# Optimization experiments

Measured on AMD Instinct MI355X. Metric: run time of the kernel, lower is better.

Reference implementation:

```python
import jax, jax.numpy as jnp
import numpy as np

N = 100000      # nodes
E = 1_600_000   # edges
IN = 128        # in_channels
HID = 32        # hidden_channels (per head)
HEADS = 4
NC = 10         # num_classes
NEG_SLOPE = 0.2 # GATConv leaky relu slope
BN_EPS = 1e-5


def _gat_conv(x, src, dst, W, a_src, a_dst, bias, heads, out_ch, concat):
    # x: [N, F_in]; W: [F_in, heads*out_ch]; a_src/a_dst: [heads, out_ch]
    n = x.shape[0]
    h = (x @ W).reshape(n, heads, out_ch)                    # [N,H,C]
    al_src = jnp.sum(h * a_src, axis=-1)                     # [N,H]
    al_dst = jnp.sum(h * a_dst, axis=-1)                     # [N,H]
    e = jax.nn.leaky_relu(al_src[src] + al_dst[dst], NEG_SLOPE)  # [E,H]
    # segment softmax over destination node
    m = jax.ops.segment_max(e, dst, num_segments=n)          # [N,H]
    ex = jnp.exp(e - m[dst])
    s = jax.ops.segment_sum(ex, dst, num_segments=n)         # [N,H]
    alpha = ex / (s[dst] + 1e-16)                            # [E,H]
    out = jax.ops.segment_sum(h[src] * alpha[:, :, None], dst, num_segments=n)  # [N,H,C]
    if concat:
        out = out.reshape(n, heads * out_ch)
    else:
        out = out.mean(axis=1)
    return out + bias


def _bn(x, gamma, beta, mean, var):
    # eval-mode BatchNorm1d with running stats
    return (x - mean) * jax.lax.rsqrt(var + BN_EPS) * gamma + beta


def setup_inputs() -> dict:
    key = jax.random.key(0)
    ks = iter(jax.random.split(key, 40))
    d = {}
    d['x'] = jax.random.normal(next(ks), (N, IN), dtype=jnp.float32)
    d['edge_index'] = jax.random.randint(next(ks), (2, E), 0, N, dtype=jnp.int32)
    dims = [(IN, HID, HEADS), (HID * HEADS, HID, HEADS), (HID * HEADS, HID, 1)]
    for i, (fin, c, h) in enumerate(dims):
        d[f'W{i}'] = jax.random.normal(next(ks), (fin, h * c), dtype=jnp.float32) * (1.0 / np.sqrt(fin))
        d[f'as{i}'] = jax.random.normal(next(ks), (h, c), dtype=jnp.float32) * 0.1
        d[f'ad{i}'] = jax.random.normal(next(ks), (h, c), dtype=jnp.float32) * 0.1
        bdim = h * c if i < 2 else c
        d[f'b{i}'] = jnp.zeros((bdim,), dtype=jnp.float32)
        d[f'g{i}'] = jax.random.uniform(next(ks), (bdim,), dtype=jnp.float32, minval=0.5, maxval=1.5)
        d[f'bt{i}'] = jax.random.normal(next(ks), (bdim,), dtype=jnp.float32) * 0.1
        d[f'm{i}'] = jax.random.normal(next(ks), (bdim,), dtype=jnp.float32) * 0.1
        d[f'v{i}'] = jax.random.uniform(next(ks), (bdim,), dtype=jnp.float32, minval=0.5, maxval=1.5)
    d['Wc'] = jax.random.normal(next(ks), (HID, NC), dtype=jnp.float32) * (1.0 / np.sqrt(HID))
    d['bc'] = jnp.zeros((NC,), dtype=jnp.float32)
    return d


def reference(x, edge_index, W0, as0, ad0, b0, g0, bt0, m0, v0,
              W1, as1, ad1, b1, g1, bt1, m1, v1,
              W2, as2, ad2, b2, g2, bt2, m2, v2, Wc, bc):
    src, dst = edge_index[0], edge_index[1]
    # layer 0: concat heads
    h = _gat_conv(x, src, dst, W0, as0, ad0, b0, HEADS, HID, True)
    h = jax.nn.elu(_bn(h, g0, bt0, m0, v0))
    # layer 1: concat heads
    h = _gat_conv(h, src, dst, W1, as1, ad1, b1, HEADS, HID, True)
    h = jax.nn.elu(_bn(h, g1, bt1, m1, v1))
    # layer 2: single head, no concat
    h = _gat_conv(h, src, dst, W2, as2, ad2, b2, 1, HID, False)
    h = jax.nn.elu(_bn(h, g2, bt2, m2, v2))
    # dropout is identity in eval mode
    return h @ Wc + bc
```

## Files before the change

kernel.cpp:

```cpp
#include <hip/hip_runtime.h>
#include <hip/hip_bf16.h>
#include <math.h>

#define NN   100000
#define NE   1600000
#define FIN  128
#define HID  32
#define NHEADS 4
#define NCLS 10

typedef unsigned int uint32;
typedef __fp16 half2_t __attribute__((ext_vector_type(2)));
typedef __fp16 half8_t __attribute__((ext_vector_type(8)));
typedef float  f32x4   __attribute__((ext_vector_type(4)));
typedef uint32 u32x4   __attribute__((ext_vector_type(4)));

__device__ __forceinline__ uint32 packh2(float a, float b) {
    half2_t h = __builtin_amdgcn_cvt_pkrtz(a, b);
    return __builtin_bit_cast(uint32, h);
}
__device__ __forceinline__ float h_lo(uint32 v) {
    return (float)__builtin_bit_cast(half2_t, v)[0];
}
__device__ __forceinline__ float h_hi(uint32 v) {
    return (float)__builtin_bit_cast(half2_t, v)[1];
}
__device__ __forceinline__ half8_t as_h8(uint4 v) {
    return __builtin_bit_cast(half8_t, v);
}

__global__ void zero_i32(int* __restrict__ p, int n) {
    int i = blockIdx.x * blockDim.x + threadIdx.x;
    if (i < n) p[i] = 0;
}

__global__ void hist_rank_kernel(const int* __restrict__ dst, int* __restrict__ cnt,
                                 int* __restrict__ rank, int e) {
    const int t0 = blockIdx.x * (blockDim.x * 4) + threadIdx.x;
    int d[4];
    bool a[4];
#pragma unroll
    for (int k = 0; k < 4; ++k) {
        const int j = t0 + k * 256;
        a[k] = (j < e);
        d[k] = a[k] ? __builtin_nontemporal_load(&dst[j]) : 0;
    }
    int r[4];
#pragma unroll
    for (int k = 0; k < 4; ++k)
        if (a[k]) r[k] = atomicAdd(&cnt[d[k]], 1);
#pragma unroll
    for (int k = 0; k < 4; ++k) {
        const int j = t0 + k * 256;
        if (a[k]) __builtin_nontemporal_store(r[k], &rank[j]);
    }
}

__global__ void scan_block_sums(const int* __restrict__ cnt, int* __restrict__ bsum, int n) {
    __shared__ int sm[256];
    int i = blockIdx.x * 256 + threadIdx.x;
    int v = (i < n) ? cnt[i] : 0;
    sm[threadIdx.x] = v;
    __syncthreads();
    for (int off = 128; off > 0; off >>= 1) {
        if (threadIdx.x < off) sm[threadIdx.x] += sm[threadIdx.x + off];
        __syncthreads();
    }
    if (threadIdx.x == 0) bsum[blockIdx.x] = sm[0];
}

__global__ void scan_single(const int* __restrict__ bsum, int* __restrict__ boff, int nb) {
    __shared__ int sm[512];
    int t = threadIdx.x;
    int v = (t < nb) ? bsum[t] : 0;
    sm[t] = v;
    __syncthreads();
    for (int off = 1; off < 512; off <<= 1) {
        int u = (t >= off) ? sm[t - off] : 0;
        __syncthreads();
        sm[t] += u;
        __syncthreads();
    }
    if (t < nb) boff[t] = sm[t] - v;
}

__global__ void scan_final(const int* __restrict__ cnt, const int* __restrict__ boff,
                           int* __restrict__ rowptr, int n) {
    __shared__ int sm[256];
    int i = blockIdx.x * 256 + threadIdx.x;
    int v = (i < n) ? cnt[i] : 0;
    sm[threadIdx.x] = v;
    __syncthreads();
    for (int off = 1; off < 256; off <<= 1) {
        int u = (threadIdx.x >= off) ? sm[threadIdx.x - off] : 0;
        __syncthreads();
        sm[threadIdx.x] += u;
        __syncthreads();
    }
    int incl = sm[threadIdx.x];
    int excl = incl - v;
    if (i < n) rowptr[i] = boff[blockIdx.x] + excl;
    if (i == n - 1) rowptr[n] = boff[blockIdx.x] + incl;
}

__global__ void scatter_kernel(const int* __restrict__ src, const int* __restrict__ dst,
                               const int* __restrict__ rank, const int* __restrict__ rowptr,
                               int* __restrict__ esrc, int e) {
    const int t0 = blockIdx.x * (blockDim.x * 4) + threadIdx.x;
#pragma unroll
    for (int k = 0; k < 4; ++k) {
        const int j = t0 + k * 256;
        if (j < e) {
            const int d = __builtin_nontemporal_load(&dst[j]);
            const int s = __builtin_nontemporal_load(&src[j]);
            const int r = __builtin_nontemporal_load(&rank[j]);
            __builtin_nontemporal_store(s, &esrc[rowptr[d] + r]);
        }
    }
}

__global__ void conv_w_kernel(const float* __restrict__ W0, const float* __restrict__ W1,
                              const float* __restrict__ W2, uint32* __restrict__ Wt0,
                              uint32* __restrict__ Wt1, uint32* __restrict__ Wt2) {
    int t = blockIdx.x * blockDim.x + threadIdx.x;
    if (t < 8192) {
        const int nn = t >> 6, ku = t & 63;
        Wt0[t] = packh2(W0[(2 * ku) * 128 + nn], W0[(2 * ku + 1) * 128 + nn]);
    } else if (t < 16384) {
        const int l = t - 8192;
        const int nn = l >> 6, ku = l & 63;
        Wt1[l] = packh2(W1[(2 * ku) * 128 + nn], W1[(2 * ku + 1) * 128 + nn]);
    } else if (t < 18432) {
        const int l = t - 16384;
        const int nn = l >> 6, ku = l & 63;
        Wt2[l] = packh2(W2[(2 * ku) * 32 + nn], W2[(2 * ku + 1) * 32 + nn]);
    }
}

__global__ void bn_prep_kernel(
    const float* __restrict__ b0, const float* __restrict__ g0, const float* __restrict__ bt0,
    const float* __restrict__ m0, const float* __restrict__ v0,
    const float* __restrict__ b1, const float* __restrict__ g1, const float* __restrict__ bt1,
    const float* __restrict__ m1, const float* __restrict__ v1,
    const float* __restrict__ b2, const float* __restrict__ g2, const float* __restrict__ bt2,
    const float* __restrict__ m2, const float* __restrict__ v2,
    float* __restrict__ A, float* __restrict__ B) {
    const int t = threadIdx.x;
    const float *b, *g, *bt, *m, *v;
    int c;
    if (t < 128)      { b = b0; g = g0; bt = bt0; m = m0; v = v0; c = t; }
    else if (t < 256) { b = b1; g = g1; bt = bt1; m = m1; v = v1; c = t - 128; }
    else if (t < 288) { b = b2; g = g2; bt = bt2; m = m2; v = v2; c = t - 256; }
    else return;
    const float s = g[c] * rsqrtf(v[c] + 1e-5f);
    A[t] = s;
    B[t] = bt[c] + (b[c] - m[c]) * s;
}

template <int FOUT, int H, bool CONVA>
__global__ __launch_bounds__(256) void gemm_mfma(const void* __restrict__ Xv,
                                                 const uint32* __restrict__ Wt,
                                                 const float* __restrict__ a_s,
                                                 const float* __restrict__ a_d,
                                                 float* __restrict__ alS,
                                                 float* __restrict__ alD,
                                                 uint32* __restrict__ Outh, int n) {
    constexpr int NT = FOUT / 16;
    const int wave = threadIdx.x >> 6;
    const int lane = threadIdx.x & 63;
    const int c = lane & 15;
    const int q = lane >> 4;
    const int row0 = blockIdx.x * 128 + wave * 32;

    int r0 = row0 + c;
    int r1 = row0 + 16 + c;
    if (r0 >= n) r0 = n - 1;
    if (r1 >= n) r1 = n - 1;

    f32x4 acc[2][NT];
#pragma unroll
    for (int m = 0; m < 2; ++m)
#pragma unroll
        for (int nt = 0; nt < NT; ++nt) acc[m][nt] = (f32x4){0.f, 0.f, 0.f, 0.f};

    const uint4*  XU = (const uint4*)Xv;
    const float4* XF = (const float4*)Xv;
    const uint4*  WU = (const uint4*)Wt;

#pragma unroll
    for (int ks = 0; ks < 4; ++ks) {
        half8_t a0, a1;
        if constexpr (CONVA) {
            const float4 f0 = XF[(size_t)r0 * 32 + (ks * 4 + q) * 2];
            const float4 f1 = XF[(size_t)r0 * 32 + (ks * 4 + q) * 2 + 1];
            a0 = as_h8(make_uint4(packh2(f0.x, f0.y), packh2(f0.z, f0.w),
                                  packh2(f1.x, f1.y), packh2(f1.z, f1.w)));
            const float4 g0 = XF[(size_t)r1 * 32 + (ks * 4 + q) * 2];
            const float4 g1 = XF[(size_t)r1 * 32 + (ks * 4 + q) * 2 + 1];
            a1 = as_h8(make_uint4(packh2(g0.x, g0.y), packh2(g0.z, g0.w),
                                  packh2(g1.x, g1.y), packh2(g1.z, g1.w)));
        } else {
            a0 = as_h8(XU[(size_t)r0 * 16 + ks * 4 + q]);
            a1 = as_h8(XU[(size_t)r1 * 16 + ks * 4 + q]);
        }
#pragma unroll
        for (int nt = 0; nt < NT; ++nt) {
            const half8_t b = as_h8(WU[(nt * 16 + c) * 16 + ks * 4 + q]);
            acc[0][nt] = __builtin_amdgcn_mfma_f32_16x16x32_f16(a0, b, acc[0][nt], 0, 0, 0);
            acc[1][nt] = __builtin_amdgcn_mfma_f32_16x16x32_f16(a1, b, acc[1][nt], 0, 0, 0);
        }
    }

    float asv[NT], adv[NT];
#pragma unroll
    for (int nt = 0; nt < NT; ++nt) {
        asv[nt] = a_s[c + 16 * nt];
        adv[nt] = a_d[c + 16 * nt];
    }

#pragma unroll
    for (int m = 0; m < 2; ++m) {
#pragma unroll
        for (int reg = 0; reg < 4; ++reg) {
            const int grow = row0 + m * 16 + q * 4 + reg;
            const bool ok = (grow < n);
            if constexpr (H == 4) {
                float ps[4], pd[4];
#pragma unroll
                for (int h = 0; h < 4; ++h) {
                    ps[h] = acc[m][2 * h][reg] * asv[2 * h] + acc[m][2 * h + 1][reg] * asv[2 * h + 1];
                    pd[h] = acc[m][2 * h][reg] * adv[2 * h] + acc[m][2 * h + 1][reg] * adv[2 * h + 1];
                }
#pragma unroll
                for (int off = 1; off < 16; off <<= 1) {
#pragma unroll
                    for (int h = 0; h < 4; ++h) {
                        ps[h] += __shfl_xor(ps[h], off);
                        pd[h] += __shfl_xor(pd[h], off);
                    }
                }
                if (c < 4 && ok) {
                    const float vs = (c == 0) ? ps[0] : (c == 1) ? ps[1] : (c == 2) ? ps[2] : ps[3];
                    const float vd = (c == 0) ? pd[0] : (c == 1) ? pd[1] : (c == 2) ? pd[2] : pd[3];
                    alS[(size_t)grow * 4 + c] = vs;
                    alD[(size_t)grow * 4 + c] = vd;
                }
            } else {
                float ps = acc[m][0][reg] * asv[0] + acc[m][1][reg] * asv[1];
                float pd = acc[m][0][reg] * adv[0] + acc[m][1][reg] * adv[1];
#pragma unroll
                for (int off = 1; off < 16; off <<= 1) {
                    ps += __shfl_xor(ps, off);
                    pd += __shfl_xor(pd, off);
                }
                if (c == 0 && ok) {
                    alS[grow] = ps;
                    alD[grow] = pd;
                }
            }
#pragma unroll
            for (int nt = 0; nt < NT; ++nt) {
                const float v = acc[m][nt][reg];
                const float o = __shfl_xor(v, 1);
                if (((c & 1) == 0) && ok) {
                    Outh[(size_t)grow * (FOUT / 2) + nt * 8 + (c >> 1)] = packh2(v, o);
                }
            }
        }
    }
}

template <int H, int C>
__global__ __launch_bounds__(256) void gat_aggregate(
    const uint32* __restrict__ Hb,
    const int* __restrict__ rowptr, const int* __restrict__ esrc,
    const float* __restrict__ alS, const float* __restrict__ alD,
    const float* __restrict__ bnA, const float* __restrict__ bnB,
    uint32* __restrict__ B16, int n) {
    constexpr int F    = H * C;
    constexpr int RU4  = F / 8;
    constexpr int SLOTS = 64 / RU4;
    constexpr int UNROLL = 16 / SLOTS;

    const int wave = threadIdx.x >> 6;
    const int lane = threadIdx.x & 63;
    int d = blockIdx.x * 4 + wave;
    if (d >= n) return;
    d = __builtin_amdgcn_readfirstlane(d);

    const int li = lane & (RU4 - 1);
    const int g  = lane / RU4;
    const int head = (H == 4) ? (li >> 2) : 0;

    const float ald = alD[(size_t)d * H + head];
    const int beg = rowptr[d];
    const int end = rowptr[d + 1];
    const int endm1 = end - 1;

    float acc[8];
#pragma unroll
    for (int k = 0; k < 8; ++k) acc[k] = 0.f;
    float den = 0.f;

    const uint4* HbU4 = (const uint4*)Hb;

    for (int base = beg; base < end; base += 16) {
#pragma unroll
        for (int u = 0; u < UNROLL; ++u) {
            const int j  = base + u * SLOTS + g;
            const bool act = (j < end);
            const int jc = act ? j : endm1;
            const int sj = __builtin_nontemporal_load(&esrc[jc]);
            const float aw = (H == 4) ? alS[(size_t)sj * 4 + head] : alS[sj];
            float t = aw + ald;
            t = fmaxf(t, 0.2f * t);
            const float ex = act ? __expf(t) : 0.f;
            den += ex;
            const uint4 v = HbU4[(size_t)sj * RU4 + li];
            acc[0] = fmaf(h_lo(v.x), ex, acc[0]);
            acc[1] = fmaf(h_hi(v.x), ex, acc[1]);
            acc[2] = fmaf(h_lo(v.y), ex, acc[2]);
            acc[3] = fmaf(h_hi(v.y), ex, acc[3]);
            acc[4] = fmaf(h_lo(v.z), ex, acc[4]);
            acc[5] = fmaf(h_hi(v.z), ex, acc[5]);
            acc[6] = fmaf(h_lo(v.w), ex, acc[6]);
            acc[7] = fmaf(h_hi(v.w), ex, acc[7]);
        }
    }

#pragma unroll
    for (int off = RU4; off < 64; off <<= 1) {
#pragma unroll
        for (int k = 0; k < 8; ++k) acc[k] += __shfl_xor(acc[k], off);
        den += __shfl_xor(den, off);
    }

    if (lane < RU4) {
        const float inv = 1.f / (den + 1e-16f);
        const int c0 = 8 * li;
        const float4 A0 = *(const float4*)(bnA + c0);
        const float4 A1 = *(const float4*)(bnA + c0 + 4);
        const float4 B0 = *(const float4*)(bnB + c0);
        const float4 B1 = *(const float4*)(bnB + c0 + 4);
        const float As[8] = {A0.x, A0.y, A0.z, A0.w, A1.x, A1.y, A1.z, A1.w};
        const float Bs[8] = {B0.x, B0.y, B0.z, B0.w, B1.x, B1.y, B1.z, B1.w};
        float y[8];
#pragma unroll
        for (int k = 0; k < 8; ++k) {
            const float yy = acc[k] * inv * As[k] + Bs[k];
            y[k] = yy > 0.f ? yy : expm1f(yy);
        }
        u32x4 o;
        o.x = packh2(y[0], y[1]);
        o.y = packh2(y[2], y[3]);
        o.z = packh2(y[4], y[5]);
        o.w = packh2(y[6], y[7]);
        __builtin_nontemporal_store(o, (u32x4*)B16 + (size_t)d * RU4 + li);
    }
}

__global__ __launch_bounds__(256) void classifier_kernel(
    const uint32* __restrict__ H3, const float* __restrict__ Wc,
    const float* __restrict__ bc, float* __restrict__ out, int n) {
    const int ni = blockIdx.x * blockDim.x + threadIdx.x;
    if (ni >= n) return;
    const uint4* row = (const uint4*)(H3 + (size_t)ni * 16);
    float xf[32];
#pragma unroll
    for (int u = 0; u < 4; ++u) {
        const uint4 v = row[u];
        xf[u * 8 + 0] = h_lo(v.x); xf[u * 8 + 1] = h_hi(v.x);
        xf[u * 8 + 2] = h_lo(v.y); xf[u * 8 + 3] = h_hi(v.y);
        xf[u * 8 + 4] = h_lo(v.z); xf[u * 8 + 5] = h_hi(v.z);
        xf[u * 8 + 6] = h_lo(v.w); xf[u * 8 + 7] = h_hi(v.w);
    }
    float o[NCLS];
#pragma unroll
    for (int c = 0; c < NCLS; ++c) o[c] = bc[c];
#pragma unroll
    for (int u = 0; u < 32; ++u) {
#pragma unroll
        for (int c = 0; c < NCLS; ++c) o[c] = fmaf(xf[u], Wc[u * NCLS + c], o[c]);
    }
    float* orow = out + (size_t)ni * NCLS;
#pragma unroll
    for (int c = 0; c < NCLS; c += 2) {
        *(float2*)(orow + c) = make_float2(o[c], o[c + 1]);
    }
}

static inline char* align256(char* p) {
    return (char*)(((uintptr_t)p + 255) & ~(uintptr_t)255);
}

extern "C" void kernel_launch(void* const* d_in, const int* in_sizes, int n_in,
                              void* d_out, int out_size, void* d_ws, size_t ws_size,
                              hipStream_t stream) {
    const float* x  = (const float*)d_in[0];
    const int*   ei = (const int*)d_in[1];
    const int N = in_sizes[0] / FIN;
    const int E = in_sizes[1] / 2;
    const int* src = ei;
    const int* dst = ei + E;

    const float *W0 = (const float*)d_in[2],  *as0 = (const float*)d_in[3],
                *ad0 = (const float*)d_in[4], *b0 = (const float*)d_in[5],
                *g0 = (const float*)d_in[6],  *bt0 = (const float*)d_in[7],
                *m0 = (const float*)d_in[8],  *v0 = (const float*)d_in[9];
    const float *W1 = (const float*)d_in[10], *as1 = (const float*)d_in[11],
                *ad1 = (const float*)d_in[12],*b1 = (const float*)d_in[13],
                *g1 = (const float*)d_in[14], *bt1 = (const float*)d_in[15],
                *m1 = (const float*)d_in[16], *v1 = (const float*)d_in[17];
    const float *W2 = (const float*)d_in[18], *as2 = (const float*)d_in[19],
                *ad2 = (const float*)d_in[20],*b2 = (const float*)d_in[21],
                *g2 = (const float*)d_in[22], *bt2 = (const float*)d_in[23],
                *m2 = (const float*)d_in[24], *v2 = (const float*)d_in[25];
    const float *Wc = (const float*)d_in[26], *bc = (const float*)d_in[27];
    float* out = (float*)d_out;

    char* p = (char*)d_ws;
    uint32* Ht  = (uint32*)p;   p = align256(p + (size_t)N * 64 * 4);
    uint32* B16 = (uint32*)p;   p = align256(p + (size_t)N * 64 * 4);
    uint32* Wt0 = (uint32*)p;   p = align256(p + 8192 * 4);
    uint32* Wt1 = (uint32*)p;   p = align256(p + 8192 * 4);
    uint32* Wt2 = (uint32*)p;   p = align256(p + 2048 * 4);
    float* alS = (float*)p;     p = align256(p + (size_t)N * NHEADS * 4);
    float* alD = (float*)p;     p = align256(p + (size_t)N * NHEADS * 4);
    int* cnt = (int*)p;         p = align256(p + (size_t)N * 4);
    int* rowptr = (int*)p;      p = align256(p + (size_t)(N + 1) * 4);
    int* rank = (int*)p;        p = align256(p + (size_t)E * 4);
    int* esrc = (int*)p;        p = align256(p + (size_t)E * 4);
    int* bsum = (int*)p;        p = align256(p + 512 * 4);
    int* boff = (int*)p;        p = align256(p + 512 * 4);
    float* bnA = (float*)p;     p = align256(p + 288 * 4);
    float* bnB = (float*)p;     p = align256(p + 288 * 4);
    (void)ws_size; (void)n_in; (void)out_size;

    const int NB = (N + 255) / 256;
    const int EB4 = (E + 1023) / 1024;

    zero_i32<<<NB, 256, 0, stream>>>(cnt, N);
    hist_rank_kernel<<<EB4, 256, 0, stream>>>(dst, cnt, rank, E);
    scan_block_sums<<<NB, 256, 0, stream>>>(cnt, bsum, N);
    scan_single<<<1, 512, 0, stream>>>(bsum, boff, NB);
    scan_final<<<NB, 256, 0, stream>>>(cnt, boff, rowptr, N);
    scatter_kernel<<<EB4, 256, 0, stream>>>(src, dst, rank, rowptr, esrc, E);

    conv_w_kernel<<<72, 256, 0, stream>>>(W0, W1, W2, Wt0, Wt1, Wt2);
    bn_prep_kernel<<<1, 320, 0, stream>>>(b0, g0, bt0, m0, v0,
                                          b1, g1, bt1, m1, v1,
                                          b2, g2, bt2, m2, v2, bnA, bnB);

    const int GB = (N + 127) / 128;
    const int AB = (N + 3) / 4;

    gemm_mfma<128, 4, true><<<GB, 256, 0, stream>>>(x, Wt0, as0, ad0, alS, alD, Ht, N);
    gat_aggregate<4, 32><<<AB, 256, 0, stream>>>(Ht, rowptr, esrc, alS, alD,
                                                 bnA, bnB, B16, N);
    gemm_mfma<128, 4, false><<<GB, 256, 0, stream>>>(B16, Wt1, as1, ad1, alS, alD, Ht, N);
    gat_aggregate<4, 32><<<AB, 256, 0, stream>>>(Ht, rowptr, esrc, alS, alD,
                                                 bnA + 128, bnB + 128, B16, N);
    gemm_mfma<32, 1, false><<<GB, 256, 0, stream>>>(B16, Wt2, as2, ad2, alS, alD, Ht, N);
    gat_aggregate<1, 32><<<AB, 256, 0, stream>>>(Ht, rowptr, esrc, alS, alD,
                                                 bnA + 256, bnB + 256, B16, N);
    classifier_kernel<<<(N + 255) / 256, 256, 0, stream>>>(B16, Wc, bc, out, N);
}
```

Before: 557.9 us.

## Fuse setup kernels, drop rank array, use atomic write pointers in CSR scatter

Merges zeroing, weight conversion and BN parameter prep into one setup kernel, and folds the single-block offset scan into scan_final by having each block sum the preceding block totals. The histogram no longer records per-edge ranks; the scatter instead claims slots with atomics on a per-node write pointer, which removes the 1.6M-entry rank array and its traffic. Non-temporal loads and stores in the aggregation kernel become ordinary accesses. Edge order within each CSR row becomes nondeterministic, which can change floating-point summation order, and the scatter now contends on atomics.

```diff
diff --git a/kernel.cpp b/kernel.cpp
--- a/kernel.cpp
+++ b/kernel.cpp
@@ -13,7 +13,6 @@
 typedef __fp16 half2_t __attribute__((ext_vector_type(2)));
 typedef __fp16 half8_t __attribute__((ext_vector_type(8)));
 typedef float  f32x4   __attribute__((ext_vector_type(4)));
-typedef uint32 u32x4   __attribute__((ext_vector_type(4)));
 
 __device__ __forceinline__ uint32 packh2(float a, float b) {
     half2_t h = __builtin_amdgcn_cvt_pkrtz(a, b);
@@ -29,100 +28,20 @@
     return __builtin_bit_cast(half8_t, v);
 }
 
-__global__ void zero_i32(int* __restrict__ p, int n) {
-    int i = blockIdx.x * blockDim.x + threadIdx.x;
-    if (i < n) p[i] = 0;
-}
-
-__global__ void hist_rank_kernel(const int* __restrict__ dst, int* __restrict__ cnt,
-                                 int* __restrict__ rank, int e) {
-    const int t0 = blockIdx.x * (blockDim.x * 4) + threadIdx.x;
-    int d[4];
-    bool a[4];
-#pragma unroll
-    for (int k = 0; k < 4; ++k) {
-        const int j = t0 + k * 256;
-        a[k] = (j < e);
-        d[k] = a[k] ? __builtin_nontemporal_load(&dst[j]) : 0;
-    }
-    int r[4];
-#pragma unroll
-    for (int k = 0; k < 4; ++k)
-        if (a[k]) r[k] = atomicAdd(&cnt[d[k]], 1);
-#pragma unroll
-    for (int k = 0; k < 4; ++k) {
-        const int j = t0 + k * 256;
-        if (a[k]) __builtin_nontemporal_store(r[k], &rank[j]);
-    }
-}
-
-__global__ void scan_block_sums(const int* __restrict__ cnt, int* __restrict__ bsum, int n) {
-    __shared__ int sm[256];
-    int i = blockIdx.x * 256 + threadIdx.x;
-    int v = (i < n) ? cnt[i] : 0;
-    sm[threadIdx.x] = v;
-    __syncthreads();
-    for (int off = 128; off > 0; off >>= 1) {
-        if (threadIdx.x < off) sm[threadIdx.x] += sm[threadIdx.x + off];
-        __syncthreads();
-    }
-    if (threadIdx.x == 0) bsum[blockIdx.x] = sm[0];
-}
-
-__global__ void scan_single(const int* __restrict__ bsum, int* __restrict__ boff, int nb) {
-    __shared__ int sm[512];
-    int t = threadIdx.x;
-    int v = (t < nb) ? bsum[t] : 0;
-    sm[t] = v;
-    __syncthreads();
-    for (int off = 1; off < 512; off <<= 1) {
-        int u = (t >= off) ? sm[t - off] : 0;
-        __syncthreads();
-        sm[t] += u;
-        __syncthreads();
-    }
-    if (t < nb) boff[t] = sm[t] - v;
-}
-
-__global__ void scan_final(const int* __restrict__ cnt, const int* __restrict__ boff,
-                           int* __restrict__ rowptr, int n) {
-    __shared__ int sm[256];
-    int i = blockIdx.x * 256 + threadIdx.x;
-    int v = (i < n) ? cnt[i] : 0;
-    sm[threadIdx.x] = v;
-    __syncthreads();
-    for (int off = 1; off < 256; off <<= 1) {
-        int u = (threadIdx.x >= off) ? sm[threadIdx.x - off] : 0;
-        __syncthreads();
-        sm[threadIdx.x] += u;
-        __syncthreads();
-    }
-    int incl = sm[threadIdx.x];
-    int excl = incl - v;
-    if (i < n) rowptr[i] = boff[blockIdx.x] + excl;
-    if (i == n - 1) rowptr[n] = boff[blockIdx.x] + incl;
-}
-
-__global__ void scatter_kernel(const int* __restrict__ src, const int* __restrict__ dst,
-                               const int* __restrict__ rank, const int* __restrict__ rowptr,
-                               int* __restrict__ esrc, int e) {
-    const int t0 = blockIdx.x * (blockDim.x * 4) + threadIdx.x;
-#pragma unroll
-    for (int k = 0; k < 4; ++k) {
-        const int j = t0 + k * 256;
-        if (j < e) {
-            const int d = __builtin_nontemporal_load(&dst[j]);
-            const int s = __builtin_nontemporal_load(&src[j]);
-            const int r = __builtin_nontemporal_load(&rank[j]);
-            __builtin_nontemporal_store(s, &esrc[rowptr[d] + r]);
-        }
-    }
-}
-
-__global__ void conv_w_kernel(const float* __restrict__ W0, const float* __restrict__ W1,
-                              const float* __restrict__ W2, uint32* __restrict__ Wt0,
-                              uint32* __restrict__ Wt1, uint32* __restrict__ Wt2) {
-    int t = blockIdx.x * blockDim.x + threadIdx.x;
+__global__ __launch_bounds__(256) void setup_kernel(
+    int* __restrict__ cnt, int n,
+    const float* __restrict__ W0, const float* __restrict__ W1,
+    const float* __restrict__ W2, uint32* __restrict__ Wt0,
+    uint32* __restrict__ Wt1, uint32* __restrict__ Wt2,
+    const float* __restrict__ b0, const float* __restrict__ g0, const float* __restrict__ bt0,
+    const float* __restrict__ m0, const float* __restrict__ v0,
+    const float* __restrict__ b1, const float* __restrict__ g1, const float* __restrict__ bt1,
+    const float* __restrict__ m1, const float* __restrict__ v1,
+    const float* __restrict__ b2, const float* __restrict__ g2, const float* __restrict__ bt2,
+    const float* __restrict__ m2, const float* __restrict__ v2,
+    float* __restrict__ A, float* __restrict__ B) {
+    const int t = blockIdx.x * 256 + threadIdx.x;
+    if (t < n) cnt[t] = 0;
     if (t < 8192) {
         const int nn = t >> 6, ku = t & 63;
         Wt0[t] = packh2(W0[(2 * ku) * 128 + nn], W0[(2 * ku + 1) * 128 + nn]);
@@ -134,27 +53,88 @@
         const int l = t - 16384;
         const int nn = l >> 6, ku = l & 63;
         Wt2[l] = packh2(W2[(2 * ku) * 32 + nn], W2[(2 * ku + 1) * 32 + nn]);
-    }
-}
-
-__global__ void bn_prep_kernel(
-    const float* __restrict__ b0, const float* __restrict__ g0, const float* __restrict__ bt0,
-    const float* __restrict__ m0, const float* __restrict__ v0,
-    const float* __restrict__ b1, const float* __restrict__ g1, const float* __restrict__ bt1,
-    const float* __restrict__ m1, const float* __restrict__ v1,
-    const float* __restrict__ b2, const float* __restrict__ g2, const float* __restrict__ bt2,
-    const float* __restrict__ m2, const float* __restrict__ v2,
-    float* __restrict__ A, float* __restrict__ B) {
+    } else if (t < 18432 + 288) {
+        const int u = t - 18432;
+        const float *b, *g, *bt, *m, *v;
+        int c;
+        if (u < 128)      { b = b0; g = g0; bt = bt0; m = m0; v = v0; c = u; }
+        else if (u < 256) { b = b1; g = g1; bt = bt1; m = m1; v = v1; c = u - 128; }
+        else              { b = b2; g = g2; bt = bt2; m = m2; v = v2; c = u - 256; }
+        const float s = g[c] * rsqrtf(v[c] + 1e-5f);
+        A[u] = s;
+        B[u] = bt[c] + (b[c] - m[c]) * s;
+    }
+}
+
+__global__ void hist_kernel(const int* __restrict__ dst, int* __restrict__ cnt, int e) {
+    const int t0 = blockIdx.x * (blockDim.x * 4) + threadIdx.x;
+#pragma unroll
+    for (int k = 0; k < 4; ++k) {
+        const int j = t0 + k * 256;
+        if (j < e) atomicAdd(&cnt[dst[j]], 1);
+    }
+}
+
+__global__ void scan_block_sums(const int* __restrict__ cnt, int* __restrict__ bsum, int n) {
+    __shared__ int sm[256];
+    int i = blockIdx.x * 256 + threadIdx.x;
+    int v = (i < n) ? cnt[i] : 0;
+    sm[threadIdx.x] = v;
+    __syncthreads();
+    for (int off = 128; off > 0; off >>= 1) {
+        if (threadIdx.x < off) sm[threadIdx.x] += sm[threadIdx.x + off];
+        __syncthreads();
+    }
+    if (threadIdx.x == 0) bsum[blockIdx.x] = sm[0];
+}
+
+__global__ void scan_final(const int* __restrict__ cnt, const int* __restrict__ bsum,
+                           int* __restrict__ rowptr, int* __restrict__ wptr, int n) {
+    __shared__ int sm[256];
+    const int b = blockIdx.x;
     const int t = threadIdx.x;
-    const float *b, *g, *bt, *m, *v;
-    int c;
-    if (t < 128)      { b = b0; g = g0; bt = bt0; m = m0; v = v0; c = t; }
-    else if (t < 256) { b = b1; g = g1; bt = bt1; m = m1; v = v1; c = t - 128; }
-    else if (t < 288) { b = b2; g = g2; bt = bt2; m = m2; v = v2; c = t - 256; }
-    else return;
-    const float s = g[c] * rsqrtf(v[c] + 1e-5f);
-    A[t] = s;
-    B[t] = bt[c] + (b[c] - m[c]) * s;
+    int s = 0;
+    for (int i = t; i < b; i += 256) s += bsum[i];
+    sm[t] = s;
+    __syncthreads();
+    for (int off = 128; off > 0; off >>= 1) {
+        if (t < off) sm[t] += sm[t + off];
+        __syncthreads();
+    }
+    const int boff = sm[0];
+    __syncthreads();
+    const int i = b * 256 + t;
+    const int v = (i < n) ? cnt[i] : 0;
+    sm[t] = v;
+    __syncthreads();
+    for (int off = 1; off < 256; off <<= 1) {
+        int u = (t >= off) ? sm[t - off] : 0;
+        __syncthreads();
+        sm[t] += u;
+        __syncthreads();
+    }
+    const int incl = sm[t];
+    const int excl = incl - v;
+    if (i < n) {
+        rowptr[i] = boff + excl;
+        wptr[i]   = boff + excl;
+    }
+    if (i == n - 1) rowptr[n] = boff + incl;
+}
+
+__global__ void scatter_kernel(const int* __restrict__ src, const int* __restrict__ dst,
+                               int* __restrict__ wptr, int* __restrict__ esrc, int e) {
+    const int t0 = blockIdx.x * (blockDim.x * 4) + threadIdx.x;
+#pragma unroll
+    for (int k = 0; k < 4; ++k) {
+        const int j = t0 + k * 256;
+        if (j < e) {
+            const int d = dst[j];
+            const int s = src[j];
+            const int pos = atomicAdd(&wptr[d], 1);
+            __builtin_nontemporal_store(s, &esrc[pos]);
+        }
+    }
 }
 
 template <int FOUT, int H, bool CONVA>
@@ -310,7 +290,7 @@
             const int j  = base + u * SLOTS + g;
             const bool act = (j < end);
             const int jc = act ? j : endm1;
-            const int sj = __builtin_nontemporal_load(&esrc[jc]);
+            const int sj = esrc[jc];
             const float aw = (H == 4) ? alS[(size_t)sj * 4 + head] : alS[sj];
             float t = aw + ald;
             t = fmaxf(t, 0.2f * t);
@@ -350,12 +330,12 @@
             const float yy = acc[k] * inv * As[k] + Bs[k];
             y[k] = yy > 0.f ? yy : expm1f(yy);
         }
-        u32x4 o;
+        uint4 o;
         o.x = packh2(y[0], y[1]);
         o.y = packh2(y[2], y[3]);
         o.z = packh2(y[4], y[5]);
         o.w = packh2(y[6], y[7]);
-        __builtin_nontemporal_store(o, (u32x4*)B16 + (size_t)d * RU4 + li);
+        ((uint4*)B16)[(size_t)d * RU4 + li] = o;
     }
 }
 
@@ -428,10 +408,9 @@
     float* alD = (float*)p;     p = align256(p + (size_t)N * NHEADS * 4);
     int* cnt = (int*)p;         p = align256(p + (size_t)N * 4);
     int* rowptr = (int*)p;      p = align256(p + (size_t)(N + 1) * 4);
-    int* rank = (int*)p;        p = align256(p + (size_t)E * 4);
+    int* wptr = (int*)p;        p = align256(p + (size_t)N * 4);
     int* esrc = (int*)p;        p = align256(p + (size_t)E * 4);
     int* bsum = (int*)p;        p = align256(p + 512 * 4);
-    int* boff = (int*)p;        p = align256(p + 512 * 4);
     float* bnA = (float*)p;     p = align256(p + 288 * 4);
     float* bnB = (float*)p;     p = align256(p + 288 * 4);
     (void)ws_size; (void)n_in; (void)out_size;
@@ -439,17 +418,15 @@
     const int NB = (N + 255) / 256;
     const int EB4 = (E + 1023) / 1024;
 
-    zero_i32<<<NB, 256, 0, stream>>>(cnt, N);
-    hist_rank_kernel<<<EB4, 256, 0, stream>>>(dst, cnt, rank, E);
+    setup_kernel<<<NB, 256, 0, stream>>>(cnt, N, W0, W1, W2, Wt0, Wt1, Wt2,
+                                         b0, g0, bt0, m0, v0,
+                                         b1, g1, bt1, m1, v1,
+                                         b2, g2, bt2, m2, v2, bnA, bnB);
+
+    hist_kernel<<<EB4, 256, 0, stream>>>(dst, cnt, E);
     scan_block_sums<<<NB, 256, 0, stream>>>(cnt, bsum, N);
-    scan_single<<<1, 512, 0, stream>>>(bsum, boff, NB);
-    scan_final<<<NB, 256, 0, stream>>>(cnt, boff, rowptr, N);
-    scatter_kernel<<<EB4, 256, 0, stream>>>(src, dst, rank, rowptr, esrc, E);
-
-    conv_w_kernel<<<72, 256, 0, stream>>>(W0, W1, W2, Wt0, Wt1, Wt2);
-    bn_prep_kernel<<<1, 320, 0, stream>>>(b0, g0, bt0, m0, v0,
-                                          b1, g1, bt1, m1, v1,
-                                          b2, g2, bt2, m2, v2, bnA, bnB);
+    scan_final<<<NB, 256, 0, stream>>>(cnt, bsum, rowptr, wptr, N);
+    scatter_kernel<<<EB4, 256, 0, stream>>>(src, dst, wptr, esrc, E);
 
     const int GB = (N + 127) / 128;
     const int AB = (N + 3) / 4;
```

New measurement: 623.4 us. 11.7% more time.
